# Kernel optimization log

Measured on AMD Instinct MI355X. Metric: run time of the kernel, lower is better.

The kernel has to match this reference:

```python
import jax, jax.numpy as jnp
import numpy as np

K_NN = 10      # knn_graph(landmarks, 10)
K_HOPS = 2     # TAGConv K
DELTA_T = 10
EPS = 0.1


def knn_edges(pos, k=K_NN):
    # PyG knn_graph with loop=False, flow='source_to_target':
    # edges (src=neighbor j, dst=query i), k nearest excluding self.
    n = pos.shape[0]
    sq = jnp.sum(pos * pos, axis=-1)
    d = sq[:, None] + sq[None, :] - 2.0 * (pos @ pos.T)  # [N,N] squared dists
    d = jnp.where(jnp.eye(n, dtype=bool), jnp.inf, d)
    _, idx = jax.lax.top_k(-d, k)                        # [N,k] neighbor ids
    src = idx.reshape(-1)                                # neighbors (sources)
    dst = jnp.repeat(jnp.arange(n), k)                   # query nodes (targets)
    return src, dst


def tagconv(h, src, dst, conv_ws, conv_b):
    # out = sum_{k=0..K} (A_norm^k h) W_k + b, gcn_norm without self-loops
    n = h.shape[0]
    deg = jax.ops.segment_sum(jnp.ones_like(src, dtype=h.dtype), dst, num_segments=n)
    dinv = jnp.where(deg > 0, jax.lax.rsqrt(deg), 0.0)
    norm = dinv[src] * dinv[dst]                         # [E]
    out = h @ conv_ws[0]
    x = h
    for k in range(1, K_HOPS + 1):
        msg = x[src] * norm[:, None]                     # gather + scale [E,D]
        x = jax.ops.segment_sum(msg, dst, num_segments=n)
        out = out + x @ conv_ws[k]
    return out + conv_b


def setup_inputs() -> dict:
    key = jax.random.key(0)
    ks = jax.random.split(key, 7)
    N, D_IN, D_H, D_OUT = 8192, 3, 256, 3
    s_emb = 1.0 / np.sqrt(D_IN)
    s_h = 1.0 / np.sqrt(D_H)
    return {
        "landmarks": jax.random.normal(ks[0], (N, D_IN), jnp.float32),
        "emb_w": jax.random.normal(ks[1], (D_IN, D_H), jnp.float32) * s_emb,
        "emb_b": jax.random.normal(ks[2], (D_H,), jnp.float32) * 0.01,
        "readout_w": jax.random.normal(ks[3], (D_H, D_OUT), jnp.float32) * s_h,
        "readout_b": jax.random.normal(ks[4], (D_OUT,), jnp.float32) * 0.01,
        "conv_ws": jax.random.normal(ks[5], (K_HOPS + 1, D_H, D_H), jnp.float32) * s_h,
        "conv_b": jax.random.normal(ks[6], (D_H,), jnp.float32) * 0.01,
    }


def reference(landmarks, emb_w, emb_b, readout_w, readout_b, conv_ws, conv_b):
    src, dst = knn_edges(landmarks)
    h = landmarks @ emb_w + emb_b                        # emb
    x = h @ readout_w + readout_b                        # readout of initial state

    def step(hc, _):
        c = tagconv(hc, src, dst, conv_ws, conv_b)
        hn = hc + EPS * jnp.tanh(c)                      # Euler residual step
        return hn, hn @ readout_w + readout_b

    h_final, land_pred = jax.lax.scan(step, h, None, length=DELTA_T)
    y = h_final @ readout_w + readout_b
    return y, h_final, x, land_pred
```

## Files before the change

### kernel.cpp

```cpp
#include <hip/hip_runtime.h>
#include <float.h>
#include <math.h>

#define NN 8192
#define DH 256
#define KNN 10
#define TSTEPS 10
#define EPSC 0.1f
#define CTILE 1024
#define QPB 16

typedef short s8v __attribute__((ext_vector_type(8)));
typedef float f4v __attribute__((ext_vector_type(4)));

__device__ __forceinline__ float bf2f(unsigned short u) {
    union { unsigned u; float f; } c; c.u = ((unsigned)u) << 16; return c.f;
}
__device__ __forceinline__ unsigned short f2bf(float f) {
    union { float f; unsigned u; } c; c.f = f;
    unsigned r = c.u + 0x7FFF + ((c.u >> 16) & 1);
    return (unsigned short)(r >> 16);
}

__global__ void prep_wt(const float* __restrict__ W, unsigned short* __restrict__ Wt) {
    int e = blockIdx.x * 256 + threadIdx.x;
    int i8 = e & 7, lane = (e >> 3) & 63, nb = (e >> 9) & 15;
    int ks = (e >> 13) & 1, kc2 = (e >> 14) & 3, g = e >> 16;
    int quad = lane >> 4, l15 = lane & 15;
    int k = kc2 * 64 + ks * 32 + quad * 8 + i8;
    int n = nb * 16 + l15;
    Wt[e] = f2bf(W[g * 65536 + k * 256 + n]);
}

__global__ void prep_pos(const float* __restrict__ pos, float4* __restrict__ pos4) {
    int j = blockIdx.x * 256 + threadIdx.x;
    float x = pos[j * 3], y = pos[j * 3 + 1], z = pos[j * 3 + 2];
    float4 v; v.x = x; v.y = y; v.z = z; v.w = x * x + y * y + z * z;
    pos4[j] = v;
}

__launch_bounds__(1024)
__global__ void knn_wave(const float* __restrict__ pos, const float4* __restrict__ pos4,
                         int* __restrict__ nbr) {
    __shared__ float4 cand[CTILE];
    int tid = threadIdx.x;
    int wv = tid >> 6, lane = tid & 63;
    int i = blockIdx.x * QPB + wv;
    float xi = pos[i * 3], yi = pos[i * 3 + 1], zi = pos[i * 3 + 2];
    float sqi = xi * xi + yi * yi + zi * zi;
    int igrp = i & ~63;

    float b  = FLT_MAX;
    int   ib = -1;
    float thr = FLT_MAX;

    for (int tile = 0; tile < NN / CTILE; ++tile) {
        __syncthreads();
        cand[tid] = pos4[tile * CTILE + tid];
        __syncthreads();
#pragma unroll 4
        for (int u = 0; u < CTILE / 64; ++u) {
            int jgrp = tile * CTILE + u * 64;
            float4 c = cand[u * 64 + lane];
            int j = jgrp + lane;
            float m = c.x * xi + c.y * yi + c.z * zi;
            float d = (sqi + c.w) - 2.0f * m;
            if (jgrp == igrp) {
                if (j == i) d = FLT_MAX;
            }
            unsigned long long mask = __ballot(d < thr);
            while (mask) {
                int l = __ffsll((unsigned long long)mask) - 1;
                mask &= mask - 1;
                float dc = __int_as_float(__builtin_amdgcn_readlane(__float_as_int(d), l));
                if (dc < thr) {
                    int jc = __builtin_amdgcn_readlane(j, l);
                    float bp = __int_as_float(__builtin_amdgcn_update_dpp(
                        0, __float_as_int(b), 0x111, 0xF, 0xF, true));
                    int ip = __builtin_amdgcn_update_dpp(0, ib, 0x111, 0xF, 0xF, true);
                    bool c0 = dc < b;
                    bool cp = (lane != 0) && (dc < bp);
                    b  = c0 ? (cp ? bp : dc) : b;
                    ib = c0 ? (cp ? ip : jc) : ib;
                    thr = __int_as_float(__builtin_amdgcn_readlane(__float_as_int(b), 9));
                }
            }
        }
    }
    if (lane < KNN) nbr[i * KNN + lane] = ib;
}

__global__ void emb_kernel(const float* __restrict__ lm, const float* __restrict__ ew,
                           const float* __restrict__ eb, const float* __restrict__ rw,
                           const float* __restrict__ rb,
                           float* __restrict__ hdo, unsigned short* __restrict__ hbf,
                           float* __restrict__ xout) {
    __shared__ float s0[4], s1[4], s2[4];
    int i = blockIdx.x, d = threadIdx.x;
    float a0 = lm[i * 3], a1 = lm[i * 3 + 1], a2 = lm[i * 3 + 2];
    float h = eb[d] + a0 * ew[d] + a1 * ew[256 + d] + a2 * ew[512 + d];
    hdo[i * 256 + d] = h;
    hbf[i * 256 + d] = f2bf(h);
    float p0 = h * rw[d * 3], p1 = h * rw[d * 3 + 1], p2 = h * rw[d * 3 + 2];
    for (int off = 32; off; off >>= 1) {
        p0 += __shfl_down(p0, off, 64);
        p1 += __shfl_down(p1, off, 64);
        p2 += __shfl_down(p2, off, 64);
    }
    int lane = d & 63, wid = d >> 6;
    if (lane == 0) { s0[wid] = p0; s1[wid] = p1; s2[wid] = p2; }
    __syncthreads();
    if (d == 0) {
        xout[i * 3 + 0] = s0[0] + s0[1] + s0[2] + s0[3] + rb[0];
        xout[i * 3 + 1] = s1[0] + s1[1] + s1[2] + s1[3] + rb[1];
        xout[i * 3 + 2] = s2[0] + s2[1] + s2[2] + s2[3] + rb[2];
    }
}

__global__ void agg_kernel(const unsigned short* __restrict__ src,
                           unsigned short* __restrict__ dst,
                           const int* __restrict__ nbr) {
    int tid = threadIdx.x;
    int slot = tid >> 5, l32 = tid & 31;
    int node = blockIdx.x * 8 + slot;
    int d0 = l32 * 8;
    const int* nb = nbr + node * KNN;
    int j[KNN];
#pragma unroll
    for (int q = 0; q < KNN; q++) j[q] = nb[q];
    uint4 v[KNN];
#pragma unroll
    for (int q = 0; q < KNN; q++) v[q] = *(const uint4*)(src + j[q] * 256 + d0);
    float a[8];
#pragma unroll
    for (int e = 0; e < 8; e++) a[e] = 0.f;
#pragma unroll
    for (int q = 0; q < KNN; q++) {
        a[0] += bf2f((unsigned short)(v[q].x & 0xffff));
        a[1] += bf2f((unsigned short)(v[q].x >> 16));
        a[2] += bf2f((unsigned short)(v[q].y & 0xffff));
        a[3] += bf2f((unsigned short)(v[q].y >> 16));
        a[4] += bf2f((unsigned short)(v[q].z & 0xffff));
        a[5] += bf2f((unsigned short)(v[q].z >> 16));
        a[6] += bf2f((unsigned short)(v[q].w & 0xffff));
        a[7] += bf2f((unsigned short)(v[q].w >> 16));
    }
    uint4 o;
    o.x = (unsigned)f2bf(a[0]*0.1f) | ((unsigned)f2bf(a[1]*0.1f) << 16);
    o.y = (unsigned)f2bf(a[2]*0.1f) | ((unsigned)f2bf(a[3]*0.1f) << 16);
    o.z = (unsigned)f2bf(a[4]*0.1f) | ((unsigned)f2bf(a[5]*0.1f) << 16);
    o.w = (unsigned)f2bf(a[6]*0.1f) | ((unsigned)f2bf(a[7]*0.1f) << 16);
    *(uint4*)(dst + node * 256 + d0) = o;
}

__launch_bounds__(512, 4)
__global__ void gemm_step(unsigned short* hbf,
                          const unsigned short* __restrict__ x1,
                          const int* __restrict__ nbr,
                          const unsigned short* __restrict__ Wt,
                          const float* __restrict__ cb,
                          const float* __restrict__ rw, const float* __restrict__ rb,
                          float* hdo, float* __restrict__ yout, float* yfin) {
    __shared__ __align__(16) short Ah[16 * 264];
    __shared__ __align__(16) short A1[16 * 264];
    __shared__ __align__(16) short X2[16 * 264];
    __shared__ float rwl[768];
    __shared__ float cbl[256];
    __shared__ float yred[8][4][4][3];

    int tid = threadIdx.x;
    int m0 = blockIdx.x * 16;
    for (int idx = tid; idx < 768; idx += 512) rwl[idx] = rw[idx];
    if (tid < 256) cbl[tid] = cb[tid];

    int w = tid >> 6, lane = tid & 63;
    int quad = lane >> 4, l15 = lane & 15;
    int row = tid >> 5, cg = tid & 31;

    {
        uint4 va = *(const uint4*)(((const unsigned short*)hbf) + (m0 + row) * 256 + cg * 8);
        *(uint4*)((unsigned short*)&Ah[row * 264 + cg * 8]) = va;
        uint4 vb = *(const uint4*)(x1 + (m0 + row) * 256 + cg * 8);
        *(uint4*)((unsigned short*)&A1[row * 264 + cg * 8]) = vb;
    }
    {
        const int* nb = nbr + (m0 + row) * KNN;
        int j[KNN];
#pragma unroll
        for (int q = 0; q < KNN; q++) j[q] = nb[q];
        float a[8];
#pragma unroll
        for (int e = 0; e < 8; e++) a[e] = 0.f;
#pragma unroll
        for (int q = 0; q < KNN; q++) {
            uint4 v = *(const uint4*)(x1 + j[q] * 256 + cg * 8);
            a[0] += bf2f((unsigned short)(v.x & 0xffff));
            a[1] += bf2f((unsigned short)(v.x >> 16));
            a[2] += bf2f((unsigned short)(v.y & 0xffff));
            a[3] += bf2f((unsigned short)(v.y >> 16));
            a[4] += bf2f((unsigned short)(v.z & 0xffff));
            a[5] += bf2f((unsigned short)(v.z >> 16));
            a[6] += bf2f((unsigned short)(v.w & 0xffff));
            a[7] += bf2f((unsigned short)(v.w >> 16));
        }
        uint4 o;
        o.x = (unsigned)f2bf(a[0]*0.1f) | ((unsigned)f2bf(a[1]*0.1f) << 16);
        o.y = (unsigned)f2bf(a[2]*0.1f) | ((unsigned)f2bf(a[3]*0.1f) << 16);
        o.z = (unsigned)f2bf(a[4]*0.1f) | ((unsigned)f2bf(a[5]*0.1f) << 16);
        o.w = (unsigned)f2bf(a[6]*0.1f) | ((unsigned)f2bf(a[7]*0.1f) << 16);
        *(uint4*)((unsigned short*)&X2[row * 264 + cg * 8]) = o;
    }
    __syncthreads();

    f4v acc[2];
    acc[0] = (f4v){0.f, 0.f, 0.f, 0.f};
    acc[1] = (f4v){0.f, 0.f, 0.f, 0.f};

#pragma unroll
    for (int kc = 0; kc < 12; kc++) {
        const short* Ab = (kc < 4) ? Ah : (kc < 8) ? A1 : X2;
        int kl = (kc & 3) * 64;
#pragma unroll
        for (int ks = 0; ks < 2; ks++) {
            s8v a = *(const s8v*)(&Ab[l15 * 264 + kl + ks * 32 + quad * 8]);
#pragma unroll
            for (int f = 0; f < 2; f++) {
                s8v b = *(const s8v*)(Wt + ((kc * 2 + ks) * 16 + (w * 2 + f)) * 512 + lane * 8);
                acc[f] = __builtin_amdgcn_mfma_f32_16x16x32_bf16(a, b, acc[f], 0, 0, 0);
            }
        }
    }

    float py[4][3] = {};
#pragma unroll
    for (int f = 0; f < 2; f++) {
        int col = w * 32 + f * 16 + l15;
        float cbv = cbl[col];
        float rw0 = rwl[col * 3], rw1 = rwl[col * 3 + 1], rw2 = rwl[col * 3 + 2];
#pragma unroll
        for (int r = 0; r < 4; r++) {
            int grow = m0 + quad * 4 + r;
            float cval = acc[f][r] + cbv;
            float hn = hdo[grow * 256 + col] + EPSC * tanhf(cval);
            hdo[grow * 256 + col] = hn;
            hbf[grow * 256 + col] = f2bf(hn);
            py[r][0] += hn * rw0; py[r][1] += hn * rw1; py[r][2] += hn * rw2;
        }
    }
    for (int off = 1; off < 16; off <<= 1)
        for (int r = 0; r < 4; r++)
            for (int j = 0; j < 3; j++)
                py[r][j] += __shfl_xor(py[r][j], off, 64);
    if (l15 == 0)
        for (int r = 0; r < 4; r++)
            for (int j = 0; j < 3; j++)
                yred[w][quad][r][j] = py[r][j];
    __syncthreads();
    if (w == 0 && l15 == 0) {
        for (int r = 0; r < 4; r++) {
            int grow = m0 + quad * 4 + r;
            for (int j = 0; j < 3; j++) {
                float yv = rb[j];
                for (int ww = 0; ww < 8; ww++) yv += yred[ww][quad][r][j];
                yout[grow * 3 + j] = yv;
                if (yfin) yfin[grow * 3 + j] = yv;
            }
        }
    }
}

extern "C" void kernel_launch(void* const* d_in, const int* in_sizes, int n_in,
                              void* d_out, int out_size, void* d_ws, size_t ws_size,
                              hipStream_t stream) {
    const float* lm = (const float*)d_in[0];
    const float* ew = (const float*)d_in[1];
    const float* eb = (const float*)d_in[2];
    const float* rw = (const float*)d_in[3];
    const float* rb = (const float*)d_in[4];
    const float* cw = (const float*)d_in[5];
    const float* cb = (const float*)d_in[6];

    float* out = (float*)d_out;
    float* y_out = out;
    float* h_out = out + 24576;
    float* x_out = out + 24576 + 2097152;
    float* lp_out = x_out + 24576;

    char* ws = (char*)d_ws;
    int* nbr = (int*)ws;                       ws += NN * KNN * sizeof(int);
    float4* pos4 = (float4*)ws;                ws += NN * sizeof(float4);
    char* uni = ws;
    unsigned short* hbf = (unsigned short*)uni;
    unsigned short* x1  = hbf + NN * DH;
    unsigned short* Wt  = x1 + NN * DH;

    prep_pos<<<NN / 256, 256, 0, stream>>>(lm, pos4);
    knn_wave<<<NN / QPB, 1024, 0, stream>>>(lm, pos4, nbr);
    prep_wt<<<768, 256, 0, stream>>>(cw, Wt);
    emb_kernel<<<NN, 256, 0, stream>>>(lm, ew, eb, rw, rb, h_out, hbf, x_out);
    for (int t = 0; t < TSTEPS; t++) {
        agg_kernel<<<NN / 8, 256, 0, stream>>>(hbf, x1, nbr);
        gemm_step<<<NN / 16, 512, 0, stream>>>(hbf, x1, nbr, Wt, cb, rw, rb, h_out,
                                               lp_out + t * 24576,
                                               (t == TSTEPS - 1) ? y_out : nullptr);
    }
}
```

Measured before the change: 380.1 us.

## Process 32 rows per gemm_step block to reuse weight fragments across two row tiles

Doubles the gemm_step row tile from 16 to 32 nodes, so each wave loads each weight fragment once and applies it to two 16-row MFMA tiles. This halves total weight reads from global/L2 and halves the block count. The load, aggregation and epilogue stages are reworked so each thread handles 16 columns, and launch bounds drop to 2 blocks per CU. In exchange there is more register and LDS use per block and only 256 blocks, which may reduce occupancy and latency hiding.

```diff
diff --git a/kernel.cpp b/kernel.cpp
--- a/kernel.cpp
+++ b/kernel.cpp
@@ -153,7 +153,7 @@
     *(uint4*)(dst + node * 256 + d0) = o;
 }
 
-__launch_bounds__(512, 4)
+__launch_bounds__(512, 2)
 __global__ void gemm_step(unsigned short* hbf,
                           const unsigned short* __restrict__ x1,
                           const int* __restrict__ nbr,
@@ -161,60 +161,81 @@
                           const float* __restrict__ cb,
                           const float* __restrict__ rw, const float* __restrict__ rb,
                           float* hdo, float* __restrict__ yout, float* yfin) {
-    __shared__ __align__(16) short Ah[16 * 264];
-    __shared__ __align__(16) short A1[16 * 264];
-    __shared__ __align__(16) short X2[16 * 264];
+    __shared__ __align__(16) short Ah[32 * 264];
+    __shared__ __align__(16) short A1[32 * 264];
+    __shared__ __align__(16) short X2[32 * 264];
     __shared__ float rwl[768];
     __shared__ float cbl[256];
-    __shared__ float yred[8][4][4][3];
+    __shared__ float yred[8][2][4][4][3];
 
     int tid = threadIdx.x;
-    int m0 = blockIdx.x * 16;
+    int m0 = blockIdx.x * 32;
     for (int idx = tid; idx < 768; idx += 512) rwl[idx] = rw[idx];
     if (tid < 256) cbl[tid] = cb[tid];
 
     int w = tid >> 6, lane = tid & 63;
     int quad = lane >> 4, l15 = lane & 15;
-    int row = tid >> 5, cg = tid & 31;
+    int row = tid >> 4, cg = tid & 15;
 
     {
-        uint4 va = *(const uint4*)(((const unsigned short*)hbf) + (m0 + row) * 256 + cg * 8);
-        *(uint4*)((unsigned short*)&Ah[row * 264 + cg * 8]) = va;
-        uint4 vb = *(const uint4*)(x1 + (m0 + row) * 256 + cg * 8);
-        *(uint4*)((unsigned short*)&A1[row * 264 + cg * 8]) = vb;
+        const unsigned short* hsrc = ((const unsigned short*)hbf) + (m0 + row) * 256 + cg * 16;
+        uint4 va0 = *(const uint4*)(hsrc);
+        uint4 va1 = *(const uint4*)(hsrc + 8);
+        *(uint4*)((unsigned short*)&Ah[row * 264 + cg * 16]) = va0;
+        *(uint4*)((unsigned short*)&Ah[row * 264 + cg * 16 + 8]) = va1;
+        const unsigned short* xsrc = x1 + (m0 + row) * 256 + cg * 16;
+        uint4 vb0 = *(const uint4*)(xsrc);
+        uint4 vb1 = *(const uint4*)(xsrc + 8);
+        *(uint4*)((unsigned short*)&A1[row * 264 + cg * 16]) = vb0;
+        *(uint4*)((unsigned short*)&A1[row * 264 + cg * 16 + 8]) = vb1;
     }
     {
         const int* nb = nbr + (m0 + row) * KNN;
         int j[KNN];
 #pragma unroll
         for (int q = 0; q < KNN; q++) j[q] = nb[q];
-        float a[8];
-#pragma unroll
-        for (int e = 0; e < 8; e++) a[e] = 0.f;
+        float a[16];
+#pragma unroll
+        for (int e = 0; e < 16; e++) a[e] = 0.f;
 #pragma unroll
         for (int q = 0; q < KNN; q++) {
-            uint4 v = *(const uint4*)(x1 + j[q] * 256 + cg * 8);
-            a[0] += bf2f((unsigned short)(v.x & 0xffff));
-            a[1] += bf2f((unsigned short)(v.x >> 16));
-            a[2] += bf2f((unsigned short)(v.y & 0xffff));
-            a[3] += bf2f((unsigned short)(v.y >> 16));
-            a[4] += bf2f((unsigned short)(v.z & 0xffff));
-            a[5] += bf2f((unsigned short)(v.z >> 16));
-            a[6] += bf2f((unsigned short)(v.w & 0xffff));
-            a[7] += bf2f((unsigned short)(v.w >> 16));
-        }
-        uint4 o;
-        o.x = (unsigned)f2bf(a[0]*0.1f) | ((unsigned)f2bf(a[1]*0.1f) << 16);
-        o.y = (unsigned)f2bf(a[2]*0.1f) | ((unsigned)f2bf(a[3]*0.1f) << 16);
-        o.z = (unsigned)f2bf(a[4]*0.1f) | ((unsigned)f2bf(a[5]*0.1f) << 16);
-        o.w = (unsigned)f2bf(a[6]*0.1f) | ((unsigned)f2bf(a[7]*0.1f) << 16);
-        *(uint4*)((unsigned short*)&X2[row * 264 + cg * 8]) = o;
+            const unsigned short* p = x1 + j[q] * 256 + cg * 16;
+            uint4 v0 = *(const uint4*)(p);
+            uint4 v1 = *(const uint4*)(p + 8);
+            a[0]  += bf2f((unsigned short)(v0.x & 0xffff));
+            a[1]  += bf2f((unsigned short)(v0.x >> 16));
+            a[2]  += bf2f((unsigned short)(v0.y & 0xffff));
+            a[3]  += bf2f((unsigned short)(v0.y >> 16));
+            a[4]  += bf2f((unsigned short)(v0.z & 0xffff));
+            a[5]  += bf2f((unsigned short)(v0.z >> 16));
+            a[6]  += bf2f((unsigned short)(v0.w & 0xffff));
+            a[7]  += bf2f((unsigned short)(v0.w >> 16));
+            a[8]  += bf2f((unsigned short)(v1.x & 0xffff));
+            a[9]  += bf2f((unsigned short)(v1.x >> 16));
+            a[10] += bf2f((unsigned short)(v1.y & 0xffff));
+            a[11] += bf2f((unsigned short)(v1.y >> 16));
+            a[12] += bf2f((unsigned short)(v1.z & 0xffff));
+            a[13] += bf2f((unsigned short)(v1.z >> 16));
+            a[14] += bf2f((unsigned short)(v1.w & 0xffff));
+            a[15] += bf2f((unsigned short)(v1.w >> 16));
+        }
+        uint4 o0, o1;
+        o0.x = (unsigned)f2bf(a[0]*0.1f)  | ((unsigned)f2bf(a[1]*0.1f)  << 16);
+        o0.y = (unsigned)f2bf(a[2]*0.1f)  | ((unsigned)f2bf(a[3]*0.1f)  << 16);
+        o0.z = (unsigned)f2bf(a[4]*0.1f)  | ((unsigned)f2bf(a[5]*0.1f)  << 16);
+        o0.w = (unsigned)f2bf(a[6]*0.1f)  | ((unsigned)f2bf(a[7]*0.1f)  << 16);
+        o1.x = (unsigned)f2bf(a[8]*0.1f)  | ((unsigned)f2bf(a[9]*0.1f)  << 16);
+        o1.y = (unsigned)f2bf(a[10]*0.1f) | ((unsigned)f2bf(a[11]*0.1f) << 16);
+        o1.z = (unsigned)f2bf(a[12]*0.1f) | ((unsigned)f2bf(a[13]*0.1f) << 16);
+        o1.w = (unsigned)f2bf(a[14]*0.1f) | ((unsigned)f2bf(a[15]*0.1f) << 16);
+        *(uint4*)((unsigned short*)&X2[row * 264 + cg * 16]) = o0;
+        *(uint4*)((unsigned short*)&X2[row * 264 + cg * 16 + 8]) = o1;
     }
     __syncthreads();
 
-    f4v acc[2];
-    acc[0] = (f4v){0.f, 0.f, 0.f, 0.f};
-    acc[1] = (f4v){0.f, 0.f, 0.f, 0.f};
+    f4v acc[4];
+#pragma unroll
+    for (int z = 0; z < 4; z++) acc[z] = (f4v){0.f, 0.f, 0.f, 0.f};
 
 #pragma unroll
     for (int kc = 0; kc < 12; kc++) {
@@ -222,48 +243,57 @@
         int kl = (kc & 3) * 64;
 #pragma unroll
         for (int ks = 0; ks < 2; ks++) {
-            s8v a = *(const s8v*)(&Ab[l15 * 264 + kl + ks * 32 + quad * 8]);
+            s8v a0 = *(const s8v*)(&Ab[l15 * 264 + kl + ks * 32 + quad * 8]);
+            s8v a1 = *(const s8v*)(&Ab[(16 + l15) * 264 + kl + ks * 32 + quad * 8]);
 #pragma unroll
             for (int f = 0; f < 2; f++) {
                 s8v b = *(const s8v*)(Wt + ((kc * 2 + ks) * 16 + (w * 2 + f)) * 512 + lane * 8);
-                acc[f] = __builtin_amdgcn_mfma_f32_16x16x32_bf16(a, b, acc[f], 0, 0, 0);
-            }
-        }
-    }
-
-    float py[4][3] = {};
-#pragma unroll
-    for (int f = 0; f < 2; f++) {
-        int col = w * 32 + f * 16 + l15;
-        float cbv = cbl[col];
-        float rw0 = rwl[col * 3], rw1 = rwl[col * 3 + 1], rw2 = rwl[col * 3 + 2];
-#pragma unroll
-        for (int r = 0; r < 4; r++) {
-            int grow = m0 + quad * 4 + r;
-            float cval = acc[f][r] + cbv;
-            float hn = hdo[grow * 256 + col] + EPSC * tanhf(cval);
-            hdo[grow * 256 + col] = hn;
-            hbf[grow * 256 + col] = f2bf(hn);
-            py[r][0] += hn * rw0; py[r][1] += hn * rw1; py[r][2] += hn * rw2;
+                acc[f]     = __builtin_amdgcn_mfma_f32_16x16x32_bf16(a0, b, acc[f], 0, 0, 0);
+                acc[2 + f] = __builtin_amdgcn_mfma_f32_16x16x32_bf16(a1, b, acc[2 + f], 0, 0, 0);
+            }
+        }
+    }
+
+    float py[2][4][3] = {};
+#pragma unroll
+    for (int rt = 0; rt < 2; rt++) {
+#pragma unroll
+        for (int f = 0; f < 2; f++) {
+            int col = w * 32 + f * 16 + l15;
+            float cbv = cbl[col];
+            float rw0 = rwl[col * 3], rw1 = rwl[col * 3 + 1], rw2 = rwl[col * 3 + 2];
+#pragma unroll
+            for (int r = 0; r < 4; r++) {
+                int grow = m0 + rt * 16 + quad * 4 + r;
+                float cval = acc[rt * 2 + f][r] + cbv;
+                float hn = hdo[grow * 256 + col] + EPSC * tanhf(cval);
+                hdo[grow * 256 + col] = hn;
+                hbf[grow * 256 + col] = f2bf(hn);
+                py[rt][r][0] += hn * rw0; py[rt][r][1] += hn * rw1; py[rt][r][2] += hn * rw2;
+            }
         }
     }
     for (int off = 1; off < 16; off <<= 1)
-        for (int r = 0; r < 4; r++)
-            for (int j = 0; j < 3; j++)
-                py[r][j] += __shfl_xor(py[r][j], off, 64);
+        for (int rt = 0; rt < 2; rt++)
+            for (int r = 0; r < 4; r++)
+                for (int j = 0; j < 3; j++)
+                    py[rt][r][j] += __shfl_xor(py[rt][r][j], off, 64);
     if (l15 == 0)
-        for (int r = 0; r < 4; r++)
-            for (int j = 0; j < 3; j++)
-                yred[w][quad][r][j] = py[r][j];
+        for (int rt = 0; rt < 2; rt++)
+            for (int r = 0; r < 4; r++)
+                for (int j = 0; j < 3; j++)
+                    yred[w][rt][quad][r][j] = py[rt][r][j];
     __syncthreads();
     if (w == 0 && l15 == 0) {
-        for (int r = 0; r < 4; r++) {
-            int grow = m0 + quad * 4 + r;
-            for (int j = 0; j < 3; j++) {
-                float yv = rb[j];
-                for (int ww = 0; ww < 8; ww++) yv += yred[ww][quad][r][j];
-                yout[grow * 3 + j] = yv;
-                if (yfin) yfin[grow * 3 + j] = yv;
+        for (int rt = 0; rt < 2; rt++) {
+            for (int r = 0; r < 4; r++) {
+                int grow = m0 + rt * 16 + quad * 4 + r;
+                for (int j = 0; j < 3; j++) {
+                    float yv = rb[j];
+                    for (int ww = 0; ww < 8; ww++) yv += yred[ww][rt][quad][r][j];
+                    yout[grow * 3 + j] = yv;
+                    if (yfin) yfin[grow * 3 + j] = yv;
+                }
             }
         }
     }
@@ -300,7 +330,7 @@
     emb_kernel<<<NN, 256, 0, stream>>>(lm, ew, eb, rw, rb, h_out, hbf, x_out);
     for (int t = 0; t < TSTEPS; t++) {
         agg_kernel<<<NN / 8, 256, 0, stream>>>(hbf, x1, nbr);
-        gemm_step<<<NN / 16, 512, 0, stream>>>(hbf, x1, nbr, Wt, cb, rw, rb, h_out,
+        gemm_step<<<NN / 32, 512, 0, stream>>>(hbf, x1, nbr, Wt, cb, rw, rb, h_out,
                                                lp_out + t * 24576,
                                                (t == TSTEPS - 1) ? y_out : nullptr);
     }
```

Measured after the change: 418.2 us. 10.0% more time.

## Split each KNN query across two waves and merge partial top-k lists

Applied to the files above, without the earlier changes.

Each query point is now handled by two wavefronts, each scanning half of the candidate set from a double-sized shared tile. At the end, the second wave's top-10 list goes through shared memory and is merged into the first wave's sorted list with the same DPP insertion step. This halves the serial scan per query and doubles the block count, at the cost of the merge, an extra barrier, and each half starting from a looser threshold, so more insertions happen.

```diff
diff --git a/kernel.cpp b/kernel.cpp
--- a/kernel.cpp
+++ b/kernel.cpp
@@ -8,7 +8,7 @@
 #define TSTEPS 10
 #define EPSC 0.1f
 #define CTILE 1024
-#define QPB 16
+#define QPB 8
 
 typedef short s8v __attribute__((ext_vector_type(8)));
 typedef float f4v __attribute__((ext_vector_type(4)));
@@ -42,9 +42,13 @@
 __launch_bounds__(1024)
 __global__ void knn_wave(const float* __restrict__ pos, const float4* __restrict__ pos4,
                          int* __restrict__ nbr) {
-    __shared__ float4 cand[CTILE];
+    __shared__ float4 cand[2 * CTILE];
+    __shared__ float md[QPB][KNN];
+    __shared__ int   mj[QPB][KNN];
     int tid = threadIdx.x;
-    int wv = tid >> 6, lane = tid & 63;
+    int wv = tid >> 7;
+    int half = (tid >> 6) & 1;
+    int lane = tid & 63;
     int i = blockIdx.x * QPB + wv;
     float xi = pos[i * 3], yi = pos[i * 3 + 1], zi = pos[i * 3 + 2];
     float sqi = xi * xi + yi * yi + zi * zi;
@@ -54,14 +58,17 @@
     int   ib = -1;
     float thr = FLT_MAX;
 
-    for (int tile = 0; tile < NN / CTILE; ++tile) {
+    for (int tp = 0; tp < 4; ++tp) {
         __syncthreads();
-        cand[tid] = pos4[tile * CTILE + tid];
+        cand[tid]        = pos4[tp * CTILE + tid];
+        cand[1024 + tid] = pos4[(tp + 4) * CTILE + tid];
         __syncthreads();
+        int jbase = (tp + half * 4) * CTILE;
+        const float4* cbase = cand + half * CTILE;
 #pragma unroll 4
         for (int u = 0; u < CTILE / 64; ++u) {
-            int jgrp = tile * CTILE + u * 64;
-            float4 c = cand[u * 64 + lane];
+            int jgrp = jbase + u * 64;
+            float4 c = cbase[u * 64 + lane];
             int j = jgrp + lane;
             float m = c.x * xi + c.y * yi + c.z * zi;
             float d = (sqi + c.w) - 2.0f * m;
@@ -87,7 +94,27 @@
             }
         }
     }
-    if (lane < KNN) nbr[i * KNN + lane] = ib;
+
+    __syncthreads();
+    if (half == 1 && lane < KNN) { md[wv][lane] = b; mj[wv][lane] = ib; }
+    __syncthreads();
+    if (half == 0) {
+        for (int q = 0; q < KNN; q++) {
+            float dq = md[wv][q];
+            int   jq = mj[wv][q];
+            if (dq < thr) {
+                float bp = __int_as_float(__builtin_amdgcn_update_dpp(
+                    0, __float_as_int(b), 0x111, 0xF, 0xF, true));
+                int ip = __builtin_amdgcn_update_dpp(0, ib, 0x111, 0xF, 0xF, true);
+                bool c0 = dq < b;
+                bool cp = (lane != 0) && (dq < bp);
+                b  = c0 ? (cp ? bp : dq) : b;
+                ib = c0 ? (cp ? ip : jq) : ib;
+                thr = __int_as_float(__builtin_amdgcn_readlane(__float_as_int(b), 9));
+            }
+        }
+        if (lane < KNN) nbr[i * KNN + lane] = ib;
+    }
 }
 
 __global__ void emb_kernel(const float* __restrict__ lm, const float* __restrict__ ew,
```

Result: slower. 395.5 us (+4.1%).
